# Performance work log

Measured on AMD Instinct MI355X. Metric: run time of the kernel, lower is better.

The kernel has to match this reference:

```python
import jax, jax.numpy as jnp
import numpy as np

BINS = 16
EDGE_KS = 11
EDGE_SIGMA = 1.5
EPS = 1e-9


def _gauss1d(ks, sigma):
    x = jnp.arange(ks, dtype=jnp.float32) - (ks - 1) / 2.0
    g = jnp.exp(-(x * x) / (2.0 * sigma * sigma))
    return g / jnp.sum(g)


def _conv2d(x, k):
    # x: [B,Cin,H,W], k: [Cout,Cin,kh,kw], VALID padding
    return jax.lax.conv_general_dilated(x, k, (1, 1), 'VALID',
                                        dimension_numbers=('NCHW', 'OIHW', 'NCHW'))


def _gaussian_blur(x, ks, sigma):
    g = _gauss1d(ks, sigma)
    k = jnp.outer(g, g)[None, None]  # [1,1,ks,ks]
    p = ks // 2
    xp = jnp.pad(x, ((0, 0), (0, 0), (p, p), (p, p)), mode='reflect')
    return _conv2d(xp, k)


# 8 neighbor offsets ordered by angle 0,45,...,315 (kornia canny convention)
_OFFS = [(0, 1), (1, 1), (1, 0), (1, -1), (0, -1), (-1, -1), (-1, 0), (-1, 1)]


def _dir_kernels(center, nbr):
    ks = np.zeros((8, 1, 3, 3), np.float32)
    for i, (dy, dx) in enumerate(_OFFS):
        ks[i, 0, 1, 1] = center
        ks[i, 0, 1 + dy, 1 + dx] = nbr
    return jnp.asarray(ks)


NMS_K = _dir_kernels(1.0, -1.0)   # center minus directional neighbor
HYST_K = _dir_kernels(0.0, 1.0)   # directional neighbor value
SOBEL = jnp.asarray(np.stack([
    np.array([[-1, 0, 1], [-2, 0, 2], [-1, 0, 1]], np.float32),
    np.array([[-1, -2, -1], [0, 0, 0], [1, 2, 1]], np.float32)])[:, None])  # [2,1,3,3]


def _canny_edges(gray, low=0.1, high=0.2):
    blurred = _gaussian_blur(gray, 5, 1.0)
    gp = jnp.pad(blurred, ((0, 0), (0, 0), (1, 1), (1, 1)), mode='edge')
    grads = _conv2d(gp, SOBEL)                       # [B,2,H,W]
    gx, gy = grads[:, :1], grads[:, 1:]
    mag = jnp.sqrt(gx * gx + gy * gy + 1e-6)
    ang = jnp.round(jnp.rad2deg(jnp.arctan2(gy, gx)) / 45.0)
    pos_i = jnp.mod(ang, 8).astype(jnp.int32)        # [B,1,H,W]
    neg_i = jnp.mod(ang + 4, 8).astype(jnp.int32)
    mp = jnp.pad(mag, ((0, 0), (0, 0), (1, 1), (1, 1)))
    nms = _conv2d(mp, NMS_K)                         # [B,8,H,W]
    pos = jnp.take_along_axis(nms, pos_i, axis=1)
    neg = jnp.take_along_axis(nms, neg_i, axis=1)
    mag = mag * (jnp.minimum(pos, neg) > 0.0)
    edges = (mag > low).astype(jnp.float32) * 0.5 + (mag > high).astype(jnp.float32) * 0.5

    def body(c):
        e, _ = c
        weak = (e == 0.5).astype(jnp.float32)
        strong = (e == 1.0).astype(jnp.float32)
        nb = _conv2d(jnp.pad(e, ((0, 0), (0, 0), (1, 1), (1, 1))), HYST_K)
        hm = jnp.any(nb == 1.0, axis=1, keepdims=True).astype(jnp.float32) * weak + strong
        return (hm + (hm == 0.0) * weak * 0.5, e)

    def cond(c):
        e, old = c
        return jnp.any(e != old)

    edges, _ = jax.lax.while_loop(cond, body, (edges, -jnp.ones_like(edges)))
    return (edges == 1.0).astype(jnp.float32)


def _normalize_map(m):
    B = m.shape[0]
    f = m.reshape(B, -1)
    mn = f.min(axis=1).reshape(B, 1, 1, 1)
    mx = f.max(axis=1).reshape(B, 1, 1, 1)
    return (m - mn) / (mx - mn + EPS)


def _srd(x_norm, mean, std, alpha, beta):
    B, C, H, W = x_norm.shape
    x = jnp.clip(x_norm * std + mean, 0.0, 1.0)
    gray = 0.299 * x[:, :1] + 0.587 * x[:, 1:2] + 0.114 * x[:, 2:3]
    edges = _canny_edges(gray)
    edge_density = _gaussian_blur(edges, EDGE_KS, EDGE_SIGMA)
    # per-image color histogram sparsity, batched via offset indices
    qc = jnp.round(x * (BINS - 1)).astype(jnp.int32)
    combined = qc[:, 0] * BINS * BINS + qc[:, 1] * BINS + qc[:, 2]   # [B,H,W]
    nbins = BINS ** 3
    flat = combined.reshape(B, -1) + (jnp.arange(B, dtype=jnp.int32) * nbins)[:, None]
    counts = jnp.zeros(B * nbins, jnp.float32).at[flat.reshape(-1)].add(1.0)
    probs = counts / float(H * W)
    sparsity = -jnp.log(probs[flat] + EPS).reshape(B, 1, H, W)
    fused = alpha * _normalize_map(edge_density) + beta * _normalize_map(sparsity)
    return jax.nn.sigmoid(fused)


def setup_inputs():
    key = jax.random.key(0)
    x_norm = jax.random.normal(key, (16, 3, 512, 512), jnp.float32)
    mean = jnp.array([0.485, 0.456, 0.406], jnp.float32).reshape(1, 3, 1, 1)
    std = jnp.array([0.229, 0.224, 0.225], jnp.float32).reshape(1, 3, 1, 1)
    return {'x_norm': x_norm, 'mean': mean, 'std': std,
            'alpha': jnp.float32(1.0), 'beta': jnp.float32(1.0)}


def reference(x_norm, mean, std, alpha, beta):
    return _srd(x_norm, mean, std, alpha, beta)
```

## Files before the change

kernel.cpp:

```cpp
#include <hip/hip_runtime.h>
#include <stdint.h>

#define NB 16
#define HH 512
#define WW 512
#define HW (HH*WW)
#define NBINS 4096

typedef unsigned long long u64;

__device__ __forceinline__ float clip01(float v){ return fminf(fmaxf(v, 0.0f), 1.0f); }
__device__ __forceinline__ int refl(int i, int n){ if (i < 0) i = -i; if (i >= n) i = 2*n - 2 - i; return i; }
__device__ __forceinline__ int clampi(int i, int lo, int hi){ return i < lo ? lo : (i > hi ? hi : i); }

__global__ void k_zero(uint4* __restrict__ hist4){
  int idx = blockIdx.x * 256 + threadIdx.x;
  hist4[idx] = make_uint4(0u, 0u, 0u, 0u);
}

__global__ void k_prep(const float* __restrict__ x, const float* __restrict__ mean,
                       const float* __restrict__ stdv, float* __restrict__ gray,
                       uint16_t* __restrict__ comb, uint32_t* __restrict__ hist)
{
#pragma clang fp contract(off)
  __shared__ uint32_t h[NBINS];
  for (int i = threadIdx.x; i < NBINS; i += 256) h[i] = 0u;
  __syncthreads();
  int img  = blockIdx.x >> 6;
  int base = (blockIdx.x & 63) * 4096;
  float m0 = mean[0], m1 = mean[1], m2 = mean[2];
  float s0 = stdv[0], s1 = stdv[1], s2 = stdv[2];
  const float* xb = x + (size_t)img * 3 * HW;
  float*     gb   = gray + (size_t)img*HW;
  uint16_t*  cb   = comb + (size_t)img*HW;
  #pragma unroll
  for (int it = 0; it < 4; it++){
    int f4 = it*256 + threadIdx.x;
    int p  = base + f4*4;
    float4 r = *(const float4*)(xb + p);
    float4 g = *(const float4*)(xb + HW + p);
    float4 b = *(const float4*)(xb + 2*HW + p);
    float xr[4] = {r.x, r.y, r.z, r.w};
    float xg[4] = {g.x, g.y, g.z, g.w};
    float xbl[4] = {b.x, b.y, b.z, b.w};
    float gy[4]; uint16_t cc[4];
    #pragma unroll
    for (int j = 0; j < 4; j++){
      float cr = clip01(xr[j]*s0 + m0);
      float cg = clip01(xg[j]*s1 + m1);
      float cbv= clip01(xbl[j]*s2 + m2);
      gy[j] = 0.299f*cr + 0.587f*cg + 0.114f*cbv;
      int c = ((int)rintf(cr*15.0f))*256 + ((int)rintf(cg*15.0f))*16 + (int)rintf(cbv*15.0f);
      cc[j] = (uint16_t)c;
      atomicAdd(&h[c], 1u);
    }
    *(float4*)(gb + p) = make_float4(gy[0], gy[1], gy[2], gy[3]);
    ushort4 cv; cv.x = cc[0]; cv.y = cc[1]; cv.z = cc[2]; cv.w = cc[3];
    *(ushort4*)(cb + p) = cv;
  }
  __syncthreads();
  uint32_t* gh = hist + img * NBINS;
  for (int i = threadIdx.x; i < NBINS; i += 256){ uint32_t v = h[i]; if (v) atomicAdd(&gh[i], v); }
}

__global__ void __launch_bounds__(256) k_canny(const float* __restrict__ gray,
                                               u64* __restrict__ A, u64* __restrict__ Sb)
{
#pragma clang fp contract(off)
  __shared__ float ubuf[40*73];
  __shared__ float blr[36*69];
  __shared__ uint8_t sdir[32*64];
  int b = blockIdx.x;
  int img = b >> 7;
  int t = b & 127;
  int y0 = (t >> 3) << 5;
  int x0 = (t & 7) << 6;
  const float* gb = gray + (size_t)img*HW;
  int tid = threadIdx.x;
  float g5[5]; { float s=0.0f; for(int i=0;i<5;i++){ float tt=(float)i-2.0f; g5[i]=expf(-(tt*tt)/2.0f); s+=g5[i]; } for(int i=0;i<5;i++) g5[i]/=s; }
  for (int i = tid; i < 40*72; i += 256){
    int ly = i/72, lx = i - ly*72;
    int gy = refl(y0 - 4 + ly, HH);
    int gx = refl(x0 - 4 + lx, WW);
    ubuf[ly*73 + lx] = gb[gy*WW + gx];
  }
  __syncthreads();
  for (int task = tid; task < 272; task += 256){
    int lx = task % 68;
    int ly = (task / 68) * 9;
    float w[5][5];
    #pragma unroll
    for (int j = 0; j < 4; j++)
      #pragma unroll
      for (int k = 0; k < 5; k++)
        w[j][k] = ubuf[(ly+j)*73 + lx + k];
    #pragma unroll
    for (int s = 0; s < 9; s++){
      #pragma unroll
      for (int k = 0; k < 5; k++) w[4][k] = ubuf[(ly+s+4)*73 + lx + k];
      float acc = 0.0f;
      #pragma unroll
      for (int ky = 0; ky < 5; ky++)
        #pragma unroll
        for (int kx = 0; kx < 5; kx++)
          acc += (g5[ky]*g5[kx]) * w[ky][kx];
      blr[(ly+s)*69 + lx] = acc;
      #pragma unroll
      for (int j = 0; j < 4; j++)
        #pragma unroll
        for (int k = 0; k < 5; k++) w[j][k] = w[j+1][k];
    }
  }
  __syncthreads();
  for (int i = tid; i < 34*66; i += 256){
    int ly = i/66, lx = i - ly*66;
    int Y = y0 - 1 + ly, X = x0 - 1 + lx;
    float m = 0.0f;
    if (Y >= 0 && Y < HH && X >= 0 && X < WW){
      float v[3][3];
      for (int dy = 0; dy < 3; dy++){
        int Yl = clampi(Y + dy - 1, 0, HH-1) - (y0 - 2);
        for (int dx = 0; dx < 3; dx++){
          int Xl = clampi(X + dx - 1, 0, WW-1) - (x0 - 2);
          v[dy][dx] = blr[Yl*69 + Xl];
        }
      }
      float gx = (v[0][2] - v[0][0]) + 2.0f*(v[1][2] - v[1][0]) + (v[2][2] - v[2][0]);
      float gy = (v[2][0] + 2.0f*v[2][1] + v[2][2]) - (v[0][0] + 2.0f*v[0][1] + v[0][2]);
      m = sqrtf(gx*gx + gy*gy + 1e-6f);
      if (ly >= 1 && ly <= 32 && lx >= 1 && lx <= 64){
        float ax = fabsf(gx), ay = fabsf(gy);
        int d;
        if (ay <= 0.41421356237309503f*ax) d = (gx >= 0.0f) ? 0 : 4;
        else if (ay >= 2.4142135623730951f*ax) d = (gy > 0.0f) ? 2 : 6;
        else if (gx > 0.0f) d = (gy > 0.0f) ? 1 : 7;
        else d = (gy > 0.0f) ? 3 : 5;
        sdir[(ly-1)*64 + (lx-1)] = (uint8_t)d;
      }
    }
    ubuf[ly*67 + lx] = m;
  }
  __syncthreads();
  const int OY[8] = {0,1,1,1,0,-1,-1,-1};
  const int OX[8] = {1,1,0,-1,-1,-1,0,1};
  int lane = tid & 63, wv = tid >> 6;
  for (int j = 0; j < 8; j++){
    int y = j*4 + wv;
    int x = lane;
    float m = ubuf[(y+1)*67 + (x+1)];
    int d  = sdir[y*64 + x];
    int d2 = (d + 4) & 7;
    float mp = 0.0f, mn = 0.0f;
    { int yy=y+OY[d],  xx=x+OX[d];  int gy=y0+yy, gx=x0+xx; if(gy>=0&&gy<HH&&gx>=0&&gx<WW) mp = ubuf[(yy+1)*67 + (xx+1)]; }
    { int yy=y+OY[d2], xx=x+OX[d2]; int gy=y0+yy, gx=x0+xx; if(gy>=0&&gy<HH&&gx>=0&&gx<WW) mn = ubuf[(yy+1)*67 + (xx+1)]; }
    bool keep = ((m - mp) > 0.0f) && ((m - mn) > 0.0f);
    float mf = keep ? m : 0.0f;
    bool strong = mf > 0.2f;
    bool weak   = (mf > 0.1f) && !strong;
    u64 wb = __ballot(weak);
    u64 sb = __ballot(strong);
    if (lane == 0){
      int gy = y0 + y;
      A [img*4096 + gy*8 + (x0>>6)] = wb;
      Sb[img*4096 + gy*8 + (x0>>6)] = sb;
    }
  }
}

__device__ __forceinline__ u64 ks_flood(u64 g, u64 P){
  u64 p1 = P, g1 = g;
  g1 |= p1 & (g1 << 1);  p1 &= (p1 << 1);
  g1 |= p1 & (g1 << 2);  p1 &= (p1 << 2);
  g1 |= p1 & (g1 << 4);  p1 &= (p1 << 4);
  g1 |= p1 & (g1 << 8);  p1 &= (p1 << 8);
  g1 |= p1 & (g1 << 16); p1 &= (p1 << 16);
  g1 |= p1 & (g1 << 32);
  u64 p2 = P, g2 = g;
  g2 |= p2 & (g2 >> 1);  p2 &= (p2 >> 1);
  g2 |= p2 & (g2 >> 2);  p2 &= (p2 >> 2);
  g2 |= p2 & (g2 >> 4);  p2 &= (p2 >> 4);
  g2 |= p2 & (g2 >> 8);  p2 &= (p2 >> 8);
  g2 |= p2 & (g2 >> 16); p2 &= (p2 >> 16);
  g2 |= p2 & (g2 >> 32);
  return g1 | g2;
}

#define HROW(m, l, r_) ((m) | ((m)<<1) | ((m)>>1) | ((l)>>63) | ((r_)<<63))

#define UPD(i) do{ \
    u64 pend = Pr[i] & ~Sr[i]; \
    if (pend){ \
      u64 Sv = Sr[i]; \
      int r = r0 + (i); \
      u64 mu = ((i) > 0) ? Sr[(i)-1] : (r > 0   ? sS[(r-1)*9+w] : 0ull); \
      u64 md = ((i) < 7) ? Sr[(i)+1] : (r < 511 ? sS[(r+1)*9+w] : 0ull); \
      u64 lu = (left  && r > 0)   ? sS[(r-1)*9+w-1] : 0ull; \
      u64 ru = (right && r > 0)   ? sS[(r-1)*9+w+1] : 0ull; \
      u64 lm = left  ? sS[r*9+w-1] : 0ull; \
      u64 rm = right ? sS[r*9+w+1] : 0ull; \
      u64 ldn= (left  && r < 511) ? sS[(r+1)*9+w-1] : 0ull; \
      u64 rdn= (right && r < 511) ? sS[(r+1)*9+w+1] : 0ull; \
      u64 nb = HROW(mu,lu,ru) | HROW(Sv,lm,rm) | HROW(md,ldn,rdn); \
      u64 g = Sv | (Pr[i] & nb); \
      if (g != Sv){ \
        u64 ns = ks_flood(g, Pr[i]); \
        Sr[i] = ns; sS[r*9+w] = ns; c = true; \
      } \
    } \
  } while(0)

__global__ void __launch_bounds__(512) k_hyst(const u64* __restrict__ A, u64* __restrict__ S)
{
  __shared__ u64 sS[512*9];
  int img = blockIdx.x;
  const u64* gA = A + img * 4096;
  u64*       gS = S + img * 4096;
  int tid = threadIdx.x;
  for (int i = tid; i < 4096; i += 512)
    sS[(i>>3)*9 + (i&7)] = gS[i];
  __syncthreads();
  int  w     = tid & 7;
  int  r0    = (tid >> 3) << 3;
  bool left  = (w > 0), right = (w < 7);
  u64 Sr[8], Pr[8];
  #pragma unroll
  for (int i = 0; i < 8; i++){
    Sr[i] = sS[(r0+i)*9 + w];
    Pr[i] = gA[(r0+i)*8 + w] | Sr[i];
  }
  for (;;){
    bool changed = false;
    #pragma unroll 1
    for (int it = 0; it < 32; ++it){
      bool c = false;
      #pragma unroll
      for (int i = 0; i < 8; i++) UPD(i);
      #pragma unroll
      for (int i = 7; i >= 0; i--) UPD(i);
      if (c) changed = true;
      if (!__any(c ? 1 : 0)) break;
    }
    if (!__syncthreads_or(changed ? 1 : 0)) break;
  }
  #pragma unroll
  for (int i = 0; i < 8; i++) gS[(r0+i)*8 + w] = Sr[i];
}

__global__ void __launch_bounds__(256) k_b11(const u64* __restrict__ S, float* __restrict__ out,
                                             float2* __restrict__ part)
{
#pragma clang fp contract(off)
  __shared__ u64 wds[74][3];
  __shared__ float hb[74][64];
  __shared__ float smn[4], smx[4];
  int b = blockIdx.x;
  int img = b >> 6;
  int t = b & 63;
  int y0 = (t >> 3) << 6;
  int tx = t & 7;
  int x0 = tx << 6;
  int tid = threadIdx.x;
  float g[11]; { float s=0.0f; for(int i=0;i<11;i++){ float tt=(float)i-5.0f; g[i]=expf(-(tt*tt)/4.5f); s+=g[i]; } for(int i=0;i<11;i++) g[i]/=s; }
  for (int i = tid; i < 74*3; i += 256){
    int j = i/3, widx = i - j*3;
    int gy = refl(y0 - 5 + j, HH);
    int gw = tx - 1 + widx;
    wds[j][widx] = (gw >= 0 && gw < 8) ? S[img*4096 + gy*8 + gw] : 0ull;
  }
  __syncthreads();
  for (int i = tid; i < 74*64; i += 256){
    int j = i >> 6, c = i & 63;
    float acc = 0.0f;
    for (int k = 0; k < 11; k++){
      int xx = refl(x0 + c + k - 5, WW);
      int widx = (xx >> 6) - tx + 1;
      float bv = (float)((wds[j][widx] >> (xx & 63)) & 1ull);
      acc += g[k] * bv;
    }
    hb[j][c] = acc;
  }
  __syncthreads();
  float mn = 3.4e38f, mx = -3.4e38f;
  float* ob = out + (size_t)img*HW;
  for (int i = tid; i < 4096; i += 256){
    int y = i >> 6, c = i & 63;
    float acc = 0.0f;
    for (int k = 0; k < 11; k++) acc += g[k] * hb[y + k][c];
    ob[(y0 + y)*WW + x0 + c] = acc;
    mn = fminf(mn, acc); mx = fmaxf(mx, acc);
  }
  for (int off = 32; off >= 1; off >>= 1){
    mn = fminf(mn, __shfl_down(mn, off));
    mx = fmaxf(mx, __shfl_down(mx, off));
  }
  int wv = tid >> 6, ln = tid & 63;
  if (ln == 0){ smn[wv] = mn; smx[wv] = mx; }
  __syncthreads();
  if (tid == 0){
    part[b] = make_float2(fminf(fminf(smn[0],smn[1]),fminf(smn[2],smn[3])),
                          fmaxf(fmaxf(smx[0],smx[1]),fmaxf(smx[2],smx[3])));
  }
}

__global__ void __launch_bounds__(256) k_edred(const float2* __restrict__ part,
                                               const uint32_t* __restrict__ hist,
                                               uint32_t* __restrict__ stats){
  __shared__ uint32_t sx[4], sn[4];
  int img = blockIdx.x;
  int tid = threadIdx.x;
  uint32_t mx = 0u, mn = 0xFFFFFFFFu;
  for (int i = tid; i < NBINS; i += 256){
    uint32_t c = hist[img*NBINS + i];
    if (c > mx) mx = c;
    if (c > 0u && c < mn) mn = c;
  }
  for (int off = 32; off >= 1; off >>= 1){
    uint32_t ox = (uint32_t)__shfl_down((int)mx, off);
    uint32_t on = (uint32_t)__shfl_down((int)mn, off);
    if (ox > mx) mx = ox;
    if (on < mn) mn = on;
  }
  int wv = tid >> 6, ln = tid & 63;
  if (ln == 0){ sx[wv] = mx; sn[wv] = mn; }
  float fmn = 3.4e38f, fmx = -3.4e38f;
  if (wv == 0){
    float2 v = part[img*64 + ln];
    fmn = v.x; fmx = v.y;
    for (int off = 32; off >= 1; off >>= 1){
      fmn = fminf(fmn, __shfl_down(fmn, off));
      fmx = fmaxf(fmx, __shfl_down(fmx, off));
    }
  }
  __syncthreads();
  if (tid == 0){
    uint32_t MX = max(max(sx[0],sx[1]), max(sx[2],sx[3]));
    uint32_t MN = min(min(sn[0],sn[1]), min(sn[2],sn[3]));
    stats[img*4+0] = __float_as_uint(fmn);
    stats[img*4+1] = __float_as_uint(fmx);
    stats[img*4+2] = __float_as_uint(-logf((float)MX / 262144.0f + 1e-9f));
    stats[img*4+3] = __float_as_uint(-logf((float)MN / 262144.0f + 1e-9f));
  }
}

__global__ void k_final(const float* __restrict__ ed, const uint16_t* __restrict__ comb,
                        const uint32_t* __restrict__ hist, const uint32_t* __restrict__ stats,
                        const float* __restrict__ alpha, const float* __restrict__ beta,
                        float* __restrict__ out)
{
#pragma clang fp contract(off)
  int idx = blockIdx.x * 256 + threadIdx.x;
  int img = idx >> 18;
  float a = alpha[0], b = beta[0];
  float mne = __uint_as_float(stats[img*4+0]);
  float mxe = __uint_as_float(stats[img*4+1]);
  float mns = __uint_as_float(stats[img*4+2]);
  float mxs = __uint_as_float(stats[img*4+3]);
  float e  = ed[idx];
  float sp = -logf((float)hist[img*NBINS + comb[idx]] / 262144.0f + 1e-9f);
  float en = (e  - mne) / (mxe - mne + 1e-9f);
  float sn = (sp - mns) / (mxs - mns + 1e-9f);
  float f  = a*en + b*sn;
  out[idx] = 1.0f / (1.0f + expf(-f));
}

extern "C" void kernel_launch(void* const* d_in, const int* in_sizes, int n_in,
                              void* d_out, int out_size, void* d_ws, size_t ws_size,
                              hipStream_t stream)
{
  const float* x     = (const float*)d_in[0];
  const float* mean  = (const float*)d_in[1];
  const float* stdv  = (const float*)d_in[2];
  const float* alpha = (const float*)d_in[3];
  const float* beta  = (const float*)d_in[4];
  float* out = (float*)d_out;

  char* ws = (char*)d_ws;
  float*    gray  = (float*)ws;
  uint16_t* comb  = (uint16_t*)(ws + (16u << 20));
  float2*   part  = (float2*)(ws + (24u << 20));
  uint32_t* hist  = (uint32_t*)(ws + (28u << 20));
  u64*      Ab    = (u64*)(ws + (28u << 20) + (1u << 18));
  u64*      Sb    = (u64*)(ws + (28u << 20) + (1u << 18) + (1u << 19));
  uint32_t* stats = (uint32_t*)(ws + (28u << 20) + (1u << 18) + (2u << 19));

  hipLaunchKernelGGL(k_zero,  dim3(64),    dim3(256), 0, stream, (uint4*)hist);
  hipLaunchKernelGGL(k_prep,  dim3(1024),  dim3(256), 0, stream, x, mean, stdv, gray, comb, hist);
  hipLaunchKernelGGL(k_canny, dim3(2048),  dim3(256), 0, stream, gray, Ab, Sb);
  hipLaunchKernelGGL(k_hyst,  dim3(NB),    dim3(512), 0, stream, Ab, Sb);
  hipLaunchKernelGGL(k_b11,   dim3(1024),  dim3(256), 0, stream, Sb, out, part);
  hipLaunchKernelGGL(k_edred, dim3(NB),    dim3(256), 0, stream, part, hist, stats);
  hipLaunchKernelGGL(k_final, dim3(16384), dim3(256), 0, stream, out, comb, hist, stats, alpha, beta, out);
}
```

Baseline: 138.4 us.

## Fuse grayscale into canny, overlap histogram with hysteresis in shared launch

Canny now computes the grayscale values straight from the normalized input, so the intermediate gray buffer and its write and read go away. The histogram-zeroing kernel is folded into canny. The color-quantization and histogram work moves into the same launch as the 16-block hysteresis kernel, so the otherwise idle GPU can do that work while hysteresis runs. The hysteresis inner loop now does a fixed two passes per block-wide sync instead of an early-exit per-wave loop. The cost is extra input reads for halo pixels and more block-wide syncs during hysteresis.

```diff
diff --git a/kernel.cpp b/kernel.cpp
--- a/kernel.cpp
+++ b/kernel.cpp
@@ -13,58 +13,11 @@
 __device__ __forceinline__ int refl(int i, int n){ if (i < 0) i = -i; if (i >= n) i = 2*n - 2 - i; return i; }
 __device__ __forceinline__ int clampi(int i, int lo, int hi){ return i < lo ? lo : (i > hi ? hi : i); }
 
-__global__ void k_zero(uint4* __restrict__ hist4){
-  int idx = blockIdx.x * 256 + threadIdx.x;
-  hist4[idx] = make_uint4(0u, 0u, 0u, 0u);
-}
-
-__global__ void k_prep(const float* __restrict__ x, const float* __restrict__ mean,
-                       const float* __restrict__ stdv, float* __restrict__ gray,
-                       uint16_t* __restrict__ comb, uint32_t* __restrict__ hist)
-{
-#pragma clang fp contract(off)
-  __shared__ uint32_t h[NBINS];
-  for (int i = threadIdx.x; i < NBINS; i += 256) h[i] = 0u;
-  __syncthreads();
-  int img  = blockIdx.x >> 6;
-  int base = (blockIdx.x & 63) * 4096;
-  float m0 = mean[0], m1 = mean[1], m2 = mean[2];
-  float s0 = stdv[0], s1 = stdv[1], s2 = stdv[2];
-  const float* xb = x + (size_t)img * 3 * HW;
-  float*     gb   = gray + (size_t)img*HW;
-  uint16_t*  cb   = comb + (size_t)img*HW;
-  #pragma unroll
-  for (int it = 0; it < 4; it++){
-    int f4 = it*256 + threadIdx.x;
-    int p  = base + f4*4;
-    float4 r = *(const float4*)(xb + p);
-    float4 g = *(const float4*)(xb + HW + p);
-    float4 b = *(const float4*)(xb + 2*HW + p);
-    float xr[4] = {r.x, r.y, r.z, r.w};
-    float xg[4] = {g.x, g.y, g.z, g.w};
-    float xbl[4] = {b.x, b.y, b.z, b.w};
-    float gy[4]; uint16_t cc[4];
-    #pragma unroll
-    for (int j = 0; j < 4; j++){
-      float cr = clip01(xr[j]*s0 + m0);
-      float cg = clip01(xg[j]*s1 + m1);
-      float cbv= clip01(xbl[j]*s2 + m2);
-      gy[j] = 0.299f*cr + 0.587f*cg + 0.114f*cbv;
-      int c = ((int)rintf(cr*15.0f))*256 + ((int)rintf(cg*15.0f))*16 + (int)rintf(cbv*15.0f);
-      cc[j] = (uint16_t)c;
-      atomicAdd(&h[c], 1u);
-    }
-    *(float4*)(gb + p) = make_float4(gy[0], gy[1], gy[2], gy[3]);
-    ushort4 cv; cv.x = cc[0]; cv.y = cc[1]; cv.z = cc[2]; cv.w = cc[3];
-    *(ushort4*)(cb + p) = cv;
-  }
-  __syncthreads();
-  uint32_t* gh = hist + img * NBINS;
-  for (int i = threadIdx.x; i < NBINS; i += 256){ uint32_t v = h[i]; if (v) atomicAdd(&gh[i], v); }
-}
-
-__global__ void __launch_bounds__(256) k_canny(const float* __restrict__ gray,
-                                               u64* __restrict__ A, u64* __restrict__ Sb)
+__global__ void __launch_bounds__(256) k_canny(const float* __restrict__ x,
+                                               const float* __restrict__ mean,
+                                               const float* __restrict__ stdv,
+                                               u64* __restrict__ A, u64* __restrict__ Sb,
+                                               uint4* __restrict__ hist4)
 {
 #pragma clang fp contract(off)
   __shared__ float ubuf[40*73];
@@ -75,14 +28,21 @@
   int t = b & 127;
   int y0 = (t >> 3) << 5;
   int x0 = (t & 7) << 6;
-  const float* gb = gray + (size_t)img*HW;
   int tid = threadIdx.x;
+  if (tid < 8) hist4[b*8 + tid] = make_uint4(0u,0u,0u,0u);
   float g5[5]; { float s=0.0f; for(int i=0;i<5;i++){ float tt=(float)i-2.0f; g5[i]=expf(-(tt*tt)/2.0f); s+=g5[i]; } for(int i=0;i<5;i++) g5[i]/=s; }
+  float m0 = mean[0], m1 = mean[1], m2 = mean[2];
+  float s0 = stdv[0], s1 = stdv[1], s2 = stdv[2];
+  const float* xb = x + (size_t)img * 3 * HW;
   for (int i = tid; i < 40*72; i += 256){
     int ly = i/72, lx = i - ly*72;
     int gy = refl(y0 - 4 + ly, HH);
     int gx = refl(x0 - 4 + lx, WW);
-    ubuf[ly*73 + lx] = gb[gy*WW + gx];
+    int p = gy*WW + gx;
+    float cr = clip01(xb[p]        *s0 + m0);
+    float cg = clip01(xb[HW + p]   *s1 + m1);
+    float cbv= clip01(xb[2*HW + p] *s2 + m2);
+    ubuf[ly*73 + lx] = 0.299f*cr + 0.587f*cg + 0.114f*cbv;
   }
   __syncthreads();
   for (int task = tid; task < 272; task += 256){
@@ -146,13 +106,13 @@
   int lane = tid & 63, wv = tid >> 6;
   for (int j = 0; j < 8; j++){
     int y = j*4 + wv;
-    int x = lane;
-    float m = ubuf[(y+1)*67 + (x+1)];
-    int d  = sdir[y*64 + x];
+    int xx0 = lane;
+    float m = ubuf[(y+1)*67 + (xx0+1)];
+    int d  = sdir[y*64 + xx0];
     int d2 = (d + 4) & 7;
     float mp = 0.0f, mn = 0.0f;
-    { int yy=y+OY[d],  xx=x+OX[d];  int gy=y0+yy, gx=x0+xx; if(gy>=0&&gy<HH&&gx>=0&&gx<WW) mp = ubuf[(yy+1)*67 + (xx+1)]; }
-    { int yy=y+OY[d2], xx=x+OX[d2]; int gy=y0+yy, gx=x0+xx; if(gy>=0&&gy<HH&&gx>=0&&gx<WW) mn = ubuf[(yy+1)*67 + (xx+1)]; }
+    { int yy=y+OY[d],  xx=xx0+OX[d];  int gy=y0+yy, gx=x0+xx; if(gy>=0&&gy<HH&&gx>=0&&gx<WW) mp = ubuf[(yy+1)*67 + (xx+1)]; }
+    { int yy=y+OY[d2], xx=xx0+OX[d2]; int gy=y0+yy, gx=x0+xx; if(gy>=0&&gy<HH&&gx>=0&&gx<WW) mn = ubuf[(yy+1)*67 + (xx+1)]; }
     bool keep = ((m - mp) > 0.0f) && ((m - mn) > 0.0f);
     float mf = keep ? m : 0.0f;
     bool strong = mf > 0.2f;
@@ -204,46 +164,89 @@
       u64 g = Sv | (Pr[i] & nb); \
       if (g != Sv){ \
         u64 ns = ks_flood(g, Pr[i]); \
-        Sr[i] = ns; sS[r*9+w] = ns; c = true; \
+        Sr[i] = ns; sS[r*9+w] = ns; changed = true; \
       } \
     } \
   } while(0)
 
-__global__ void __launch_bounds__(512) k_hyst(const u64* __restrict__ A, u64* __restrict__ S)
-{
-  __shared__ u64 sS[512*9];
-  int img = blockIdx.x;
-  const u64* gA = A + img * 4096;
-  u64*       gS = S + img * 4096;
+__global__ void __launch_bounds__(512) k_mid(const u64* __restrict__ A, u64* __restrict__ S,
+                                             const float* __restrict__ x,
+                                             const float* __restrict__ mean,
+                                             const float* __restrict__ stdv,
+                                             uint16_t* __restrict__ comb,
+                                             uint32_t* __restrict__ hist)
+{
+#pragma clang fp contract(off)
+  __shared__ __align__(16) char smem[512*9*8];
   int tid = threadIdx.x;
-  for (int i = tid; i < 4096; i += 512)
-    sS[(i>>3)*9 + (i&7)] = gS[i];
-  __syncthreads();
-  int  w     = tid & 7;
-  int  r0    = (tid >> 3) << 3;
-  bool left  = (w > 0), right = (w < 7);
-  u64 Sr[8], Pr[8];
-  #pragma unroll
-  for (int i = 0; i < 8; i++){
-    Sr[i] = sS[(r0+i)*9 + w];
-    Pr[i] = gA[(r0+i)*8 + w] | Sr[i];
-  }
-  for (;;){
-    bool changed = false;
-    #pragma unroll 1
-    for (int it = 0; it < 32; ++it){
-      bool c = false;
-      #pragma unroll
-      for (int i = 0; i < 8; i++) UPD(i);
-      #pragma unroll
-      for (int i = 7; i >= 0; i--) UPD(i);
-      if (c) changed = true;
-      if (!__any(c ? 1 : 0)) break;
-    }
-    if (!__syncthreads_or(changed ? 1 : 0)) break;
-  }
-  #pragma unroll
-  for (int i = 0; i < 8; i++) gS[(r0+i)*8 + w] = Sr[i];
+  if (blockIdx.x < 16){
+    u64* sS = (u64*)smem;
+    int img = blockIdx.x;
+    const u64* gA = A + img * 4096;
+    u64*       gS = S + img * 4096;
+    for (int i = tid; i < 4096; i += 512)
+      sS[(i>>3)*9 + (i&7)] = gS[i];
+    __syncthreads();
+    int  w     = tid & 7;
+    int  r0    = (tid >> 3) << 3;
+    bool left  = (w > 0), right = (w < 7);
+    u64 Sr[8], Pr[8];
+    #pragma unroll
+    for (int i = 0; i < 8; i++){
+      Sr[i] = sS[(r0+i)*9 + w];
+      Pr[i] = gA[(r0+i)*8 + w] | Sr[i];
+    }
+    for (;;){
+      bool changed = false;
+      #pragma unroll 1
+      for (int rep = 0; rep < 2; rep++){
+        #pragma unroll
+        for (int i = 0; i < 8; i++) UPD(i);
+        #pragma unroll
+        for (int i = 7; i >= 0; i--) UPD(i);
+      }
+      if (!__syncthreads_or(changed ? 1 : 0)) break;
+    }
+    #pragma unroll
+    for (int i = 0; i < 8; i++) gS[(r0+i)*8 + w] = Sr[i];
+  } else {
+    uint32_t* h = (uint32_t*)smem;
+    int pb  = blockIdx.x - 16;
+    int img = pb >> 5;
+    int base = (pb & 31) * 8192;
+    for (int i = tid; i < NBINS; i += 512) h[i] = 0u;
+    __syncthreads();
+    float m0 = mean[0], m1 = mean[1], m2 = mean[2];
+    float s0 = stdv[0], s1 = stdv[1], s2 = stdv[2];
+    const float* xb = x + (size_t)img * 3 * HW;
+    uint16_t*  cb   = comb + (size_t)img*HW;
+    #pragma unroll
+    for (int it = 0; it < 4; it++){
+      int f4 = it*512 + tid;
+      int p  = base + f4*4;
+      float4 r = *(const float4*)(xb + p);
+      float4 g = *(const float4*)(xb + HW + p);
+      float4 b = *(const float4*)(xb + 2*HW + p);
+      float xr[4] = {r.x, r.y, r.z, r.w};
+      float xg[4] = {g.x, g.y, g.z, g.w};
+      float xbl[4] = {b.x, b.y, b.z, b.w};
+      uint16_t cc[4];
+      #pragma unroll
+      for (int j = 0; j < 4; j++){
+        float cr = clip01(xr[j]*s0 + m0);
+        float cg = clip01(xg[j]*s1 + m1);
+        float cbv= clip01(xbl[j]*s2 + m2);
+        int c = ((int)rintf(cr*15.0f))*256 + ((int)rintf(cg*15.0f))*16 + (int)rintf(cbv*15.0f);
+        cc[j] = (uint16_t)c;
+        atomicAdd(&h[c], 1u);
+      }
+      ushort4 cv; cv.x = cc[0]; cv.y = cc[1]; cv.z = cc[2]; cv.w = cc[3];
+      *(ushort4*)(cb + p) = cv;
+    }
+    __syncthreads();
+    uint32_t* gh = hist + img * NBINS;
+    for (int i = tid; i < NBINS; i += 512){ uint32_t v = h[i]; if (v) atomicAdd(&gh[i], v); }
+  }
 }
 
 __global__ void __launch_bounds__(256) k_b11(const u64* __restrict__ S, float* __restrict__ out,
@@ -375,18 +378,15 @@
   float* out = (float*)d_out;
 
   char* ws = (char*)d_ws;
-  float*    gray  = (float*)ws;
-  uint16_t* comb  = (uint16_t*)(ws + (16u << 20));
-  float2*   part  = (float2*)(ws + (24u << 20));
-  uint32_t* hist  = (uint32_t*)(ws + (28u << 20));
-  u64*      Ab    = (u64*)(ws + (28u << 20) + (1u << 18));
-  u64*      Sb    = (u64*)(ws + (28u << 20) + (1u << 18) + (1u << 19));
-  uint32_t* stats = (uint32_t*)(ws + (28u << 20) + (1u << 18) + (2u << 19));
-
-  hipLaunchKernelGGL(k_zero,  dim3(64),    dim3(256), 0, stream, (uint4*)hist);
-  hipLaunchKernelGGL(k_prep,  dim3(1024),  dim3(256), 0, stream, x, mean, stdv, gray, comb, hist);
-  hipLaunchKernelGGL(k_canny, dim3(2048),  dim3(256), 0, stream, gray, Ab, Sb);
-  hipLaunchKernelGGL(k_hyst,  dim3(NB),    dim3(512), 0, stream, Ab, Sb);
+  uint16_t* comb  = (uint16_t*)ws;
+  float2*   part  = (float2*)(ws + (8u << 20));
+  uint32_t* hist  = (uint32_t*)(ws + (9u << 20));
+  u64*      Ab    = (u64*)(ws + (10u << 20));
+  u64*      Sb    = (u64*)(ws + (11u << 20));
+  uint32_t* stats = (uint32_t*)(ws + (12u << 20));
+
+  hipLaunchKernelGGL(k_canny, dim3(2048),  dim3(256), 0, stream, x, mean, stdv, Ab, Sb, (uint4*)hist);
+  hipLaunchKernelGGL(k_mid,   dim3(528),   dim3(512), 0, stream, Ab, Sb, x, mean, stdv, comb, hist);
   hipLaunchKernelGGL(k_b11,   dim3(1024),  dim3(256), 0, stream, Sb, out, part);
   hipLaunchKernelGGL(k_edred, dim3(NB),    dim3(256), 0, stream, part, hist, stats);
   hipLaunchKernelGGL(k_final, dim3(16384), dim3(256), 0, stream, out, comb, hist, stats, alpha, beta, out);
```

After: 127.8 us. 7.6% less time.
